# Kernel tuning notes

Hardware: AMD Instinct MI355X
Metric: run time of the kernel (lower is better)

## Reference

```python
import jax, jax.numpy as jnp
import numpy as np


def setup_inputs() -> dict:
    key = jax.random.key(0)
    k1, k2, k3 = jax.random.split(key, 3)
    B, L, S, H, E, D = 2, 512, 512, 8, 32, 64
    queries = jax.random.normal(k1, (B, L, H, E), dtype=jnp.float32)
    keys = jax.random.normal(k2, (B, S, H, E), dtype=jnp.float32)
    values = jax.random.normal(k3, (B, S, H, D), dtype=jnp.float32)
    v = jnp.ones((E,), dtype=jnp.float32)
    attn_mask_add = jnp.zeros((L, S), dtype=jnp.float32)
    key_lengths_add = jnp.zeros((B, S), dtype=jnp.float32)
    return {
        "queries": queries,
        "keys": keys,
        "values": values,
        "v": v,
        "attn_mask_add": attn_mask_add,
        "key_lengths_add": key_lengths_add,
    }


def reference(queries, keys, values, v, attn_mask_add, key_lengths_add):
    # Additive (Bahdanau) attention.
    # queries: (B,L,H,E), keys: (B,S,H,E), values: (B,S,H,D)
    # Broadcast add -> tanh -> contract with v: (B,L,S,H,E) -> (B,H,L,S)
    feat = jnp.tanh(queries[:, :, None, :, :] + keys[:, None, :, :, :])  # (B,L,S,H,E)
    scores = jnp.einsum("blshe,e->bhls", feat, v)  # (B,H,L,S)
    scores = scores + attn_mask_add[None, None, :, :]          # (L,S) attn mask
    scores = scores + key_lengths_add[:, None, None, :]        # (B,S) key-length mask
    A = jax.nn.softmax(scores, axis=-1)  # (B,H,L,S); dropout is identity (p=0 / eval)
    V = jnp.einsum("bhls,bshd->blhd", A, values)  # (B,L,H,D)
    return V
```

## Files before the change

kernel.cpp:

```cpp
#include <hip/hip_runtime.h>


#define BB 2
#define LL 512
#define SS 512
#define HH 8
#define EE 32
#define DD 64

#define WS_EK_OFF 0
#define WS_VT_OFF (4u * 1024u * 1024u)

typedef __attribute__((ext_vector_type(8))) short bf16x8;
typedef __attribute__((ext_vector_type(4))) float f32x4;
typedef __attribute__((ext_vector_type(4))) unsigned u32x4;

__device__ __forceinline__ unsigned short f2bf(float f) {
    unsigned u = __float_as_uint(f);
    u += 0x7FFFu + ((u >> 16) & 1u);
    return (unsigned short)(u >> 16);
}
__device__ __forceinline__ float fast_exp2(float x) {
#if __has_builtin(__builtin_amdgcn_exp2f)
    return __builtin_amdgcn_exp2f(x);
#else
    return exp2f(x);
#endif
}
__device__ __forceinline__ float fast_rcp(float x) {
    return __builtin_amdgcn_rcpf(x);
}
__device__ __forceinline__ float bcastf(float x) {
    return __int_as_float(__builtin_amdgcn_readfirstlane(__float_as_int(x)));
}

#define SCV 2.885390081777927f

__global__ __launch_bounds__(256) void prep_kernel(
    const float* __restrict__ k, const float* __restrict__ vals,
    float* __restrict__ ws)
{
    unsigned gid = blockIdx.x * 256 + threadIdx.x;
    if (gid < 32768u) {
        unsigned i  = gid;
        unsigned s  = i & 511u;
        unsigned e8 = (i >> 9) & 3u;
        unsigned h  = (i >> 11) & 7u;
        unsigned b  = i >> 14;
        const float* kr = k + (((size_t)b * SS + s) * HH + h) * EE + e8 * 8;
        float4 k0 = *(const float4*)kr;
        float4 k1 = *(const float4*)(kr + 4);
        u32x4 pk;
        pk[0] = (unsigned)f2bf(fast_exp2(SCV * k0.x)) |
                ((unsigned)f2bf(fast_exp2(SCV * k0.y)) << 16);
        pk[1] = (unsigned)f2bf(fast_exp2(SCV * k0.z)) |
                ((unsigned)f2bf(fast_exp2(SCV * k0.w)) << 16);
        pk[2] = (unsigned)f2bf(fast_exp2(SCV * k1.x)) |
                ((unsigned)f2bf(fast_exp2(SCV * k1.y)) << 16);
        pk[3] = (unsigned)f2bf(fast_exp2(SCV * k1.z)) |
                ((unsigned)f2bf(fast_exp2(SCV * k1.w)) << 16);
        ((u32x4*)((char*)ws + WS_EK_OFF))[i] = pk;
    } else {
        unsigned i      = gid - 32768u;
        unsigned lane   = i & 63u;
        unsigned c      = (i >> 6) & 15u;
        unsigned dchunk = (i >> 10) & 3u;
        unsigned h      = (i >> 12) & 7u;
        unsigned b      = i >> 15;
        unsigned qd = lane >> 4, n = lane & 15;
        unsigned d  = dchunk * 16 + n;
        unsigned s0 = c * 32 + qd * 8;
        const float* vb = vals + (((size_t)b * SS + s0) * HH + h) * DD + d;
        u32x4 pk;
        #pragma unroll
        for (int j2 = 0; j2 < 4; j2++) {
            float f0 = vb[(size_t)(2 * j2) * (HH * DD)];
            float f1 = vb[(size_t)(2 * j2 + 1) * (HH * DD)];
            pk[j2] = (unsigned)f2bf(f0) | ((unsigned)f2bf(f1) << 16);
        }
        ((u32x4*)((char*)ws + WS_VT_OFF))[i] = pk;
    }
}

__global__ __launch_bounds__(256) void addattn_kernel(
    const u32x4* __restrict__ ws_ekb,
    const bf16x8* __restrict__ ws_vtf,
    const float* __restrict__ q,
    const float* __restrict__ vvec,
    const float* __restrict__ mask,
    const float* __restrict__ klen,
    float* __restrict__ out)
{
    __shared__ u32x4 sek[4 * SS];
    __shared__ unsigned short sAb[8][SS];

    const int tid  = threadIdx.x;
    const int w    = tid >> 6;
    const int lane = tid & 63;
    const int bh   = blockIdx.x >> 6;
    const int lblk = blockIdx.x & 63;
    const int b    = bh >> 3;
    const int h    = bh & 7;
    const int l0   = lblk * 8;
    const int lw   = l0 + 2 * w;

    {
        const u32x4* esrc = ws_ekb + (size_t)bh * (4 * SS);
        #pragma unroll
        for (int t = 0; t < 8; t++)
            sek[tid + t * 256] = esrc[tid + t * 256];
    }

    float eq0[EE], eq1[EE], v2s[EE];
    {
        const float* q0 = q + (((size_t)b * LL + lw) * HH + h) * EE;
        const float* q1 = q0 + HH * EE;
        #pragma unroll
        for (int e = 0; e < EE; e += 4) {
            float4 t0 = *(const float4*)(q0 + e);
            float4 t1 = *(const float4*)(q1 + e);
            eq0[e]   = bcastf(fast_exp2(SCV * t0.x));
            eq0[e+1] = bcastf(fast_exp2(SCV * t0.y));
            eq0[e+2] = bcastf(fast_exp2(SCV * t0.z));
            eq0[e+3] = bcastf(fast_exp2(SCV * t0.w));
            eq1[e]   = bcastf(fast_exp2(SCV * t1.x));
            eq1[e+1] = bcastf(fast_exp2(SCV * t1.y));
            eq1[e+2] = bcastf(fast_exp2(SCV * t1.z));
            eq1[e+3] = bcastf(fast_exp2(SCV * t1.w));
        }
        const float4* vr = (const float4*)vvec;
        #pragma unroll
        for (int e4 = 0; e4 < EE / 4; e4++) {
            float4 t = vr[e4];
            v2s[e4*4]   = bcastf(-2.f * t.x); v2s[e4*4+1] = bcastf(-2.f * t.y);
            v2s[e4*4+2] = bcastf(-2.f * t.z); v2s[e4*4+3] = bcastf(-2.f * t.w);
        }
    }
    __syncthreads();

    float sc0[SS / 64], sc1[SS / 64];
    for (int i = 0; i < SS / 64; i++) {
        const int s = lane + i * 64;
        u32x4 g0 = sek[s];
        u32x4 g1 = sek[SS + s];
        u32x4 g2 = sek[2 * SS + s];
        u32x4 g3 = sek[3 * SS + s];
        float a0A = 0.f, a0B = 0.f, a1A = 0.f, a1B = 0.f;
        #define PAIR2(u, le, A0, A1)                                          \
        {                                                                     \
            float eklo = __uint_as_float((u) << 16);                          \
            float ekhi = __uint_as_float((u) & 0xffff0000u);                  \
            float qa0 = __builtin_fmaf(eq0[le], eklo, 1.f);                   \
            float qb0 = __builtin_fmaf(eq0[(le) + 1], ekhi, 1.f);             \
            float nm0 = __builtin_fmaf(v2s[le], qb0, v2s[(le) + 1] * qa0);    \
            A0 = __builtin_fmaf(nm0, fast_rcp(qa0 * qb0), A0);                \
            float qa1 = __builtin_fmaf(eq1[le], eklo, 1.f);                   \
            float qb1 = __builtin_fmaf(eq1[(le) + 1], ekhi, 1.f);             \
            float nm1 = __builtin_fmaf(v2s[le], qb1, v2s[(le) + 1] * qa1);    \
            A1 = __builtin_fmaf(nm1, fast_rcp(qa1 * qb1), A1);                \
        }
        PAIR2(g0[0], 0, a0A, a1A)  PAIR2(g0[1], 2, a0B, a1B)
        PAIR2(g0[2], 4, a0A, a1A)  PAIR2(g0[3], 6, a0B, a1B)
        PAIR2(g1[0], 8, a0A, a1A)  PAIR2(g1[1], 10, a0B, a1B)
        PAIR2(g1[2], 12, a0A, a1A) PAIR2(g1[3], 14, a0B, a1B)
        PAIR2(g2[0], 16, a0A, a1A) PAIR2(g2[1], 18, a0B, a1B)
        PAIR2(g2[2], 20, a0A, a1A) PAIR2(g2[3], 22, a0B, a1B)
        PAIR2(g3[0], 24, a0A, a1A) PAIR2(g3[1], 26, a0B, a1B)
        PAIR2(g3[2], 28, a0A, a1A) PAIR2(g3[3], 30, a0B, a1B)
        #undef PAIR2
        sc0[i] = a0A + a0B;
        sc1[i] = a1A + a1B;
    }

    {
        const float* kl = klen + (size_t)b * SS;
        float klv[SS / 64];
        #pragma unroll
        for (int i = 0; i < SS / 64; i++) klv[i] = kl[lane + i * 64];

        #pragma unroll
        for (int r = 0; r < 2; r++) {
            float* sc = r ? sc1 : sc0;
            const float* mrow = mask + (size_t)(lw + r) * SS;
            float ssum = 0.f;
            #pragma unroll
            for (int i = 0; i < SS / 64; i++) {
                float v = fminf(sc[i] + mrow[lane + i * 64] + klv[i], 80.f);
                sc[i] = __expf(v);
                ssum += sc[i];
            }
            #pragma unroll
            for (int off = 1; off < 64; off <<= 1) ssum += __shfl_xor(ssum, off, 64);
            float inv = fast_rcp(ssum);
            const int row = 2 * w + r;
            const int fsw = (row * 5) & 7;
            #pragma unroll
            for (int i = 0; i < SS / 64; i++) {
                int col = lane + i * 64;
                int pos = (((col >> 3) ^ fsw) << 3) | (col & 7);
                sAb[row][pos] = f2bf(sc[i] * inv);
            }
        }
    }
    __syncthreads();

    const int am  = lane & 15;
    const int qd  = lane >> 4;
    const int dof = w * 16 + am;
    const int fam = (am * 5) & 7;
    const bf16x8* vf =
        ws_vtf + ((size_t)((b * HH + h) * 4 + w) * 16) * 64 + lane;
    f32x4 acc = {0.f, 0.f, 0.f, 0.f};
    bf16x8 bv[4];
    #pragma unroll
    for (int c = 0; c < 4; c++) bv[c] = vf[c * 64];
    #pragma unroll
    for (int c = 0; c < SS / 32; c++) {
        bf16x8 af = {0, 0, 0, 0, 0, 0, 0, 0};
        if (am < 8)
            af = *(const bf16x8*)&sAb[am][((c * 4 + qd) ^ fam) << 3];
        acc = __builtin_amdgcn_mfma_f32_16x16x32_bf16(af, bv[c & 3], acc, 0, 0, 0);
        if (c + 4 < SS / 32) bv[c & 3] = vf[(c + 4) * 64];
    }
    if (qd < 2) {
        float* orow = out + (((size_t)b * LL + l0 + qd * 4) * HH + h) * DD + dof;
        #pragma unroll
        for (int r = 0; r < 4; r++)
            orow[(size_t)r * (HH * DD)] = acc[r];
    }
}

extern "C" void kernel_launch(void* const* d_in, const int* in_sizes, int n_in,
                              void* d_out, int out_size, void* d_ws, size_t ws_size,
                              hipStream_t stream) {
    const float* q    = (const float*)d_in[0];
    const float* k    = (const float*)d_in[1];
    const float* vals = (const float*)d_in[2];
    const float* vvec = (const float*)d_in[3];
    const float* mask = (const float*)d_in[4];
    const float* klen = (const float*)d_in[5];
    float* outp = (float*)d_out;

    float* ws = (float*)d_ws;
    prep_kernel<<<dim3(384), dim3(256), 0, stream>>>(k, vals, ws);

    const u32x4* ws_ekb = (const u32x4*)((char*)d_ws + WS_EK_OFF);
    const bf16x8* ws_vtf = (const bf16x8*)((char*)d_ws + WS_VT_OFF);
    addattn_kernel<<<dim3(BB * HH * (LL / 8)), dim3(256), 0, stream>>>(
        ws_ekb, ws_vtf, q, vvec, mask, klen, outp);
}
```

Before: 92.96 us.

## Split key dimension across two blocks and merge partial softmax outputs in combine kernel

Each attention block now processes half of the key sequence, writing unnormalized partial outputs and partial exp-sums to workspace, and a new combine kernel adds the halves and normalizes. This doubles the grid size and halves per-block shared memory, aiming for more parallelism and occupancy. It adds an extra kernel launch, workspace traffic, and duplicated per-block query setup.

```diff
diff --git a/kernel.cpp b/kernel.cpp
--- a/kernel.cpp
+++ b/kernel.cpp
@@ -7,9 +7,12 @@
 #define HH 8
 #define EE 32
 #define DD 64
+#define SH 256
 
 #define WS_EK_OFF 0
 #define WS_VT_OFF (4u * 1024u * 1024u)
+#define WS_PO_OFF (8u * 1024u * 1024u)
+#define WS_PS_OFF (12u * 1024u * 1024u)
 
 typedef __attribute__((ext_vector_type(8))) short bf16x8;
 typedef __attribute__((ext_vector_type(4))) float f32x4;
@@ -89,15 +92,17 @@
     const float* __restrict__ vvec,
     const float* __restrict__ mask,
     const float* __restrict__ klen,
-    float* __restrict__ out)
+    float* __restrict__ ws_po,
+    float* __restrict__ ws_ps)
 {
-    __shared__ u32x4 sek[4 * SS];
-    __shared__ unsigned short sAb[8][SS];
+    __shared__ u32x4 sek[4 * SH];
+    __shared__ unsigned short sAb[8][SH];
 
     const int tid  = threadIdx.x;
     const int w    = tid >> 6;
     const int lane = tid & 63;
-    const int bh   = blockIdx.x >> 6;
+    const int bh   = blockIdx.x >> 7;
+    const int half = (blockIdx.x >> 6) & 1;
     const int lblk = blockIdx.x & 63;
     const int b    = bh >> 3;
     const int h    = bh & 7;
@@ -105,10 +110,14 @@
     const int lw   = l0 + 2 * w;
 
     {
-        const u32x4* esrc = ws_ekb + (size_t)bh * (4 * SS);
-        #pragma unroll
-        for (int t = 0; t < 8; t++)
-            sek[tid + t * 256] = esrc[tid + t * 256];
+        const u32x4* esrc = ws_ekb + (size_t)bh * (4 * SS) + half * SH;
+        #pragma unroll
+        for (int t = 0; t < 4; t++) {
+            int idx = tid + t * 256;
+            int e8  = idx >> 8;
+            int sl  = idx & 255;
+            sek[e8 * SH + sl] = esrc[e8 * SS + sl];
+        }
     }
 
     float eq0[EE], eq1[EE], v2s[EE];
@@ -138,13 +147,13 @@
     }
     __syncthreads();
 
-    float sc0[SS / 64], sc1[SS / 64];
-    for (int i = 0; i < SS / 64; i++) {
-        const int s = lane + i * 64;
-        u32x4 g0 = sek[s];
-        u32x4 g1 = sek[SS + s];
-        u32x4 g2 = sek[2 * SS + s];
-        u32x4 g3 = sek[3 * SS + s];
+    float sc0[SH / 64], sc1[SH / 64];
+    for (int i = 0; i < SH / 64; i++) {
+        const int sl = lane + i * 64;
+        u32x4 g0 = sek[sl];
+        u32x4 g1 = sek[SH + sl];
+        u32x4 g2 = sek[2 * SH + sl];
+        u32x4 g3 = sek[3 * SH + sl];
         float a0A = 0.f, a0B = 0.f, a1A = 0.f, a1B = 0.f;
         #define PAIR2(u, le, A0, A1)                                          \
         {                                                                     \
@@ -173,33 +182,34 @@
     }
 
     {
-        const float* kl = klen + (size_t)b * SS;
-        float klv[SS / 64];
-        #pragma unroll
-        for (int i = 0; i < SS / 64; i++) klv[i] = kl[lane + i * 64];
+        const float* kl = klen + (size_t)b * SS + half * SH;
+        float klv[SH / 64];
+        #pragma unroll
+        for (int i = 0; i < SH / 64; i++) klv[i] = kl[lane + i * 64];
 
         #pragma unroll
         for (int r = 0; r < 2; r++) {
             float* sc = r ? sc1 : sc0;
-            const float* mrow = mask + (size_t)(lw + r) * SS;
+            const float* mrow = mask + (size_t)(lw + r) * SS + half * SH;
             float ssum = 0.f;
             #pragma unroll
-            for (int i = 0; i < SS / 64; i++) {
+            for (int i = 0; i < SH / 64; i++) {
                 float v = fminf(sc[i] + mrow[lane + i * 64] + klv[i], 80.f);
                 sc[i] = __expf(v);
                 ssum += sc[i];
             }
             #pragma unroll
             for (int off = 1; off < 64; off <<= 1) ssum += __shfl_xor(ssum, off, 64);
-            float inv = fast_rcp(ssum);
             const int row = 2 * w + r;
             const int fsw = (row * 5) & 7;
             #pragma unroll
-            for (int i = 0; i < SS / 64; i++) {
+            for (int i = 0; i < SH / 64; i++) {
                 int col = lane + i * 64;
                 int pos = (((col >> 3) ^ fsw) << 3) | (col & 7);
-                sAb[row][pos] = f2bf(sc[i] * inv);
+                sAb[row][pos] = f2bf(sc[i]);
             }
+            if (lane == 0)
+                ws_ps[((size_t)half * 16 + bh) * LL + lw + r] = ssum;
         }
     }
     __syncthreads();
@@ -209,25 +219,40 @@
     const int dof = w * 16 + am;
     const int fam = (am * 5) & 7;
     const bf16x8* vf =
-        ws_vtf + ((size_t)((b * HH + h) * 4 + w) * 16) * 64 + lane;
+        ws_vtf + ((size_t)(bh * 4 + w) * 16 + half * 8) * 64 + lane;
     f32x4 acc = {0.f, 0.f, 0.f, 0.f};
     bf16x8 bv[4];
     #pragma unroll
     for (int c = 0; c < 4; c++) bv[c] = vf[c * 64];
     #pragma unroll
-    for (int c = 0; c < SS / 32; c++) {
+    for (int c = 0; c < SH / 32; c++) {
         bf16x8 af = {0, 0, 0, 0, 0, 0, 0, 0};
         if (am < 8)
             af = *(const bf16x8*)&sAb[am][((c * 4 + qd) ^ fam) << 3];
         acc = __builtin_amdgcn_mfma_f32_16x16x32_bf16(af, bv[c & 3], acc, 0, 0, 0);
-        if (c + 4 < SS / 32) bv[c & 3] = vf[(c + 4) * 64];
+        if (c + 4 < SH / 32) bv[c & 3] = vf[(c + 4) * 64];
     }
     if (qd < 2) {
-        float* orow = out + (((size_t)b * LL + l0 + qd * 4) * HH + h) * DD + dof;
+        float* orow = ws_po + (((size_t)half * 16 + bh) * LL + l0 + qd * 4) * DD + dof;
         #pragma unroll
         for (int r = 0; r < 4; r++)
-            orow[(size_t)r * (HH * DD)] = acc[r];
-    }
+            orow[(size_t)r * DD] = acc[r];
+    }
+}
+
+__global__ __launch_bounds__(256) void combine_kernel(
+    const float* __restrict__ ws_po, const float* __restrict__ ws_ps,
+    float* __restrict__ out)
+{
+    unsigned gid = blockIdx.x * 256 + threadIdx.x;
+    unsigned d  = gid & 63u;
+    unsigned l  = (gid >> 6) & 511u;
+    unsigned bh = gid >> 15;
+    float o = ws_po[gid] + ws_po[(size_t)16 * LL * DD + gid];
+    float s = ws_ps[(size_t)bh * LL + l] +
+              ws_ps[(size_t)16 * LL + bh * LL + l];
+    unsigned b = bh >> 3, h = bh & 7;
+    out[(((size_t)b * LL + l) * HH + h) * DD + d] = o * fast_rcp(s);
 }
 
 extern "C" void kernel_launch(void* const* d_in, const int* in_sizes, int n_in,
@@ -246,6 +271,12 @@
 
     const u32x4* ws_ekb = (const u32x4*)((char*)d_ws + WS_EK_OFF);
     const bf16x8* ws_vtf = (const bf16x8*)((char*)d_ws + WS_VT_OFF);
-    addattn_kernel<<<dim3(BB * HH * (LL / 8)), dim3(256), 0, stream>>>(
-        ws_ekb, ws_vtf, q, vvec, mask, klen, outp);
-}
+    float* ws_po = (float*)((char*)d_ws + WS_PO_OFF);
+    float* ws_ps = (float*)((char*)d_ws + WS_PS_OFF);
+
+    addattn_kernel<<<dim3(BB * HH * 2 * (LL / 8)), dim3(256), 0, stream>>>(
+        ws_ekb, ws_vtf, q, vvec, mask, klen, ws_po, ws_ps);
+
+    combine_kernel<<<dim3((BB * HH * LL * DD) / 256), dim3(256), 0, stream>>>(
+        ws_po, ws_ps, outp);
+}
```

New measurement: 101.0 us. 1.09x slower.
